# Performance work log

Hardware: AMD Instinct MI355X
Metric: run time of the kernel (lower is better)

Reference implementation:

```python
import jax, jax.numpy as jnp
import numpy as np

N_STEPS = 20
ALPHA, BETA = 0.9, 0.8  # synaptic / membrane decay (unused given zero carried state, kept for clarity)


def _lcn_spiking_layer(h, knn, w, b):
    """h: [N, d_in]; knn: [d_out, K] indices into d_in; w: [d_out, K]; b: [1, d_out].
    Gather K neighbors per output node, weight, reduce, then snntorch Synaptic
    update with zero carried state (the source never stores returned syn/mem):
      syn = ALPHA*0 + I = I ; reset = (prev_mem > thr) = 0 ; mem = BETA*0 + syn - 0 = I
    and the layer output is mem (the source keeps the 3rd return value)."""
    g = h[:, knn]                                  # [N, d_out, K] irregular gather
    cur = jnp.sum(g * w[None, :, :], axis=2) + b   # [N, d_out]
    syn = ALPHA * jnp.zeros_like(cur) + cur
    mem = BETA * jnp.zeros_like(cur) + syn         # reset term is zero
    return mem


def setup_inputs() -> dict:
    key = jax.random.key(0)
    B, T, IN_DIM, K, OUT = 32, N_STEPS, 14400, 25, 2
    dims = [7200, 3600, 1800, 900, 450]
    ks = jax.random.split(key, 13)
    inp = {"x": jax.random.normal(ks[0], (B, T, IN_DIM), dtype=jnp.float32)}
    prev = IN_DIM
    for i, d in enumerate(dims):
        inp[f"w{i}"] = jax.random.normal(ks[1 + i], (d, K), dtype=jnp.float32) * (2.0 / K) ** 0.5
        inp[f"b{i}"] = jnp.zeros((1, d), dtype=jnp.float32)
        inp[f"knn{i}"] = jax.random.randint(ks[6 + i], (d, K), 0, prev)
        prev = d
    inp["Wfc"] = jax.random.normal(ks[11], (dims[-1], OUT), dtype=jnp.float32) * (1.0 / dims[-1]) ** 0.5
    inp["bfc"] = jnp.zeros((OUT,), dtype=jnp.float32)
    return inp


def reference(x, w0, w1, w2, w3, w4, b0, b1, b2, b3, b4, Wfc, bfc,
              knn0, knn1, knn2, knn3, knn4):
    # Source loops over 20 timesteps with independent (state never carried) work;
    # fold time into batch to vectorize, then keep the last step's angle only,
    # exactly matching the returned value of the torch forward.
    B, T, D = x.shape
    h = x.reshape(B * T, D)
    layers = ((w0, b0, knn0), (w1, b1, knn1), (w2, b2, knn2), (w3, b3, knn3), (w4, b4, knn4))
    for w, b, knn in layers:
        h = _lcn_spiking_layer(h, knn, w, b)
    angle = h @ Wfc + bfc                     # [B*T, out_dim]
    angle = angle.reshape(B, T, -1)[:, -1]    # last timestep, as in the source
    return angle
```

## Files before the change

kernel.cpp:

```cpp
#include <hip/hip_runtime.h>
#include <hip/hip_bf16.h>


#define ROWS 32
#define TSTEPS 20
#define D0 14400
#define D1 7200
#define D2 3600
#define D3 1800
#define D4 900
#define D5 450
#define KNB 25

__global__ __launch_bounds__(256)
void l0_stage(const float* __restrict__ x, float* __restrict__ h1t,
              const float* __restrict__ w, const float* __restrict__ bvec,
              const int* __restrict__ knn)
{
    __shared__ float s[D0];
    const int r = blockIdx.y;
    const float* xrow = x + ((size_t)r * TSTEPS + (TSTEPS - 1)) * (size_t)D0;

    const float4* src = reinterpret_cast<const float4*>(xrow);
    float4* dst = reinterpret_cast<float4*>(s);
#pragma unroll 1
    for (int i = threadIdx.x; i < D0 / 4; i += 256)
        dst[i] = src[i];
    __syncthreads();

    const int j0 = blockIdx.x * 900;
#pragma unroll 1
    for (int j = j0 + threadIdx.x; j < j0 + 900; j += 256) {
        const int*   kn = knn + j * KNB;
        const float* ww = w   + j * KNB;
        float acc = bvec[j];
#pragma unroll
        for (int k = 0; k < KNB; ++k)
            acc += s[kn[k]] * ww[k];
        h1t[(j << 5) + r] = acc;
    }
}

__global__ __launch_bounds__(256)
void layer_t_k(const float* __restrict__ pin, float* __restrict__ pout,
               const float* __restrict__ w, const float* __restrict__ bvec,
               const int* __restrict__ knn, int npairs)
{
    const int lane = threadIdx.x & 63;
    const int r  = lane & 31;
    const int jj = lane >> 5;
    const int nw = gridDim.x << 2;
#pragma unroll 1
    for (int jp = (blockIdx.x << 2) + (threadIdx.x >> 6); jp < npairs; jp += nw) {
        const int j = (jp << 1) + jj;
        const int*   kn = knn + j * KNB;
        const float* ww = w   + j * KNB;
        float acc = bvec[j];
#pragma unroll
        for (int k = 0; k < KNB; ++k)
            acc += pin[(kn[k] << 5) + r] * ww[k];
        pout[(j << 5) + r] = acc;
    }
}

__global__ __launch_bounds__(256)
void l4_fc(const float* __restrict__ h4t,
           const float* __restrict__ w, const float* __restrict__ bvec,
           const int* __restrict__ knn,
           const float* __restrict__ Wfc, const float* __restrict__ bfc,
           float* __restrict__ out)
{
    __shared__ float sacc[64];
    if (threadIdx.x < 64)
        sacc[threadIdx.x] = (blockIdx.x == 0) ? bfc[threadIdx.x & 1] : 0.0f;
    __syncthreads();

    const int lane = threadIdx.x & 63;
    const int r  = lane & 31;
    const int jj = lane >> 5;
    const int nw = gridDim.x << 2;
    float c0 = 0.0f, c1 = 0.0f;
#pragma unroll 1
    for (int jp = (blockIdx.x << 2) + (threadIdx.x >> 6); jp < D5 / 2; jp += nw) {
        const int j = (jp << 1) + jj;
        const int*   kn = knn + j * KNB;
        const float* ww = w   + j * KNB;
        float acc = bvec[j];
#pragma unroll
        for (int k = 0; k < KNB; ++k)
            acc += h4t[(kn[k] << 5) + r] * ww[k];
        c0 += acc * Wfc[j * 2 + 0];
        c1 += acc * Wfc[j * 2 + 1];
    }
    atomicAdd(&sacc[(r << 1) + 0], c0);
    atomicAdd(&sacc[(r << 1) + 1], c1);
    __syncthreads();
    if (threadIdx.x < 64)
        atomicAdd(&out[threadIdx.x], sacc[threadIdx.x]);
}

extern "C" void kernel_launch(void* const* d_in, const int* in_sizes, int n_in,
                              void* d_out, int out_size, void* d_ws, size_t ws_size,
                              hipStream_t stream)
{
    const float* x    = (const float*)d_in[0];
    const float* w0   = (const float*)d_in[1];
    const float* b0   = (const float*)d_in[2];
    const int*   knn0 = (const int*)  d_in[3];
    const float* w1   = (const float*)d_in[4];
    const float* b1   = (const float*)d_in[5];
    const int*   knn1 = (const int*)  d_in[6];
    const float* w2   = (const float*)d_in[7];
    const float* b2   = (const float*)d_in[8];
    const int*   knn2 = (const int*)  d_in[9];
    const float* w3   = (const float*)d_in[10];
    const float* b3   = (const float*)d_in[11];
    const int*   knn3 = (const int*)  d_in[12];
    const float* w4   = (const float*)d_in[13];
    const float* b4   = (const float*)d_in[14];
    const int*   knn4 = (const int*)  d_in[15];
    const float* Wfc  = (const float*)d_in[16];
    const float* bfc  = (const float*)d_in[17];
    float* out = (float*)d_out;

    float* h1t = (float*)d_ws;
    float* h2t = h1t + (size_t)D1 * ROWS;
    float* h3t = h2t + (size_t)D2 * ROWS;
    float* h4t = h3t + (size_t)D3 * ROWS;

    hipMemsetAsync(out, 0, (size_t)out_size * sizeof(float), stream);

    l0_stage<<<dim3(D1 / 900, ROWS), dim3(256), 0, stream>>>(x, h1t, w0, b0, knn0);

    layer_t_k<<<dim3(450), dim3(256), 0, stream>>>(h1t, h2t, w1, b1, knn1, D2 / 2);

    layer_t_k<<<dim3(225), dim3(256), 0, stream>>>(h2t, h3t, w2, b2, knn2, D3 / 2);

    layer_t_k<<<dim3(113), dim3(256), 0, stream>>>(h3t, h4t, w3, b3, knn3, D4 / 2);

    l4_fc<<<dim3(57), dim3(256), 0, stream>>>(h4t, w4, b4, knn4, Wfc, bfc, out);
}
```

Measured before the change: 131.0 us.

## Fuse layers one through four and FC into one per-row LDS-resident kernel

Replaces the four tail kernels and the output memset with a single kernel that runs one 1024-thread block per batch row. Every intermediate activation from layer 2 onward lives in shared memory, and the final FC is reduced with wave shuffles. Layer 1 output is now stored row-major so each block can load its row contiguously. This removes launch overhead and global round-trips between layers, but only 32 blocks run, which lowers parallelism, and each block re-reads all the weights and indices.

Result: slower. 138.7 us (+5.9%).

```diff
diff --git a/kernel.cpp b/kernel.cpp
--- a/kernel.cpp
+++ b/kernel.cpp
@@ -1,5 +1,4 @@
 #include <hip/hip_runtime.h>
-#include <hip/hip_bf16.h>
 
 
 #define ROWS 32
@@ -13,7 +12,7 @@
 #define KNB 25
 
 __global__ __launch_bounds__(256)
-void l0_stage(const float* __restrict__ x, float* __restrict__ h1t,
+void l0_stage(const float* __restrict__ x, float* __restrict__ h1,
               const float* __restrict__ w, const float* __restrict__ bvec,
               const int* __restrict__ knn)
 {
@@ -37,66 +36,108 @@
 #pragma unroll
         for (int k = 0; k < KNB; ++k)
             acc += s[kn[k]] * ww[k];
-        h1t[(j << 5) + r] = acc;
+        h1[(size_t)r * D1 + j] = acc;
     }
 }
 
-__global__ __launch_bounds__(256)
-void layer_t_k(const float* __restrict__ pin, float* __restrict__ pout,
-               const float* __restrict__ w, const float* __restrict__ bvec,
-               const int* __restrict__ knn, int npairs)
+__global__ __launch_bounds__(1024)
+void tail_fused(const float* __restrict__ h1,
+                const float* __restrict__ w1, const float* __restrict__ b1, const int* __restrict__ n1,
+                const float* __restrict__ w2, const float* __restrict__ b2, const int* __restrict__ n2,
+                const float* __restrict__ w3, const float* __restrict__ b3, const int* __restrict__ n3,
+                const float* __restrict__ w4, const float* __restrict__ b4, const int* __restrict__ n4,
+                const float* __restrict__ Wfc, const float* __restrict__ bfc,
+                float* __restrict__ out)
 {
-    const int lane = threadIdx.x & 63;
-    const int r  = lane & 31;
-    const int jj = lane >> 5;
-    const int nw = gridDim.x << 2;
+    __shared__ float sa[D1];
+    __shared__ float sb[D2];
+    __shared__ float sc[D3];
+    __shared__ float sd[D4];
+    __shared__ float se[D5];
+    __shared__ float red[2];
+
+    const int r   = blockIdx.x;
+    const int tid = threadIdx.x;
+
+    {
+        const float4* src = reinterpret_cast<const float4*>(h1 + (size_t)r * D1);
+        float4* dst = reinterpret_cast<float4*>(sa);
 #pragma unroll 1
-    for (int jp = (blockIdx.x << 2) + (threadIdx.x >> 6); jp < npairs; jp += nw) {
-        const int j = (jp << 1) + jj;
-        const int*   kn = knn + j * KNB;
-        const float* ww = w   + j * KNB;
-        float acc = bvec[j];
+        for (int i = tid; i < D1 / 4; i += 1024)
+            dst[i] = src[i];
+    }
+    __syncthreads();
+
+#pragma unroll 1
+    for (int j = tid; j < D2; j += 1024) {
+        const int*   kn = n1 + j * KNB;
+        const float* ww = w1 + j * KNB;
+        float acc = b1[j];
 #pragma unroll
         for (int k = 0; k < KNB; ++k)
-            acc += pin[(kn[k] << 5) + r] * ww[k];
-        pout[(j << 5) + r] = acc;
+            acc += sa[kn[k]] * ww[k];
+        sb[j] = acc;
     }
-}
-
-__global__ __launch_bounds__(256)
-void l4_fc(const float* __restrict__ h4t,
-           const float* __restrict__ w, const float* __restrict__ bvec,
-           const int* __restrict__ knn,
-           const float* __restrict__ Wfc, const float* __restrict__ bfc,
-           float* __restrict__ out)
-{
-    __shared__ float sacc[64];
-    if (threadIdx.x < 64)
-        sacc[threadIdx.x] = (blockIdx.x == 0) ? bfc[threadIdx.x & 1] : 0.0f;
     __syncthreads();
 
-    const int lane = threadIdx.x & 63;
-    const int r  = lane & 31;
-    const int jj = lane >> 5;
-    const int nw = gridDim.x << 2;
+#pragma unroll 1
+    for (int j = tid; j < D3; j += 1024) {
+        const int*   kn = n2 + j * KNB;
+        const float* ww = w2 + j * KNB;
+        float acc = b2[j];
+#pragma unroll
+        for (int k = 0; k < KNB; ++k)
+            acc += sb[kn[k]] * ww[k];
+        sc[j] = acc;
+    }
+    __syncthreads();
+
+#pragma unroll 1
+    for (int j = tid; j < D4; j += 1024) {
+        const int*   kn = n3 + j * KNB;
+        const float* ww = w3 + j * KNB;
+        float acc = b3[j];
+#pragma unroll
+        for (int k = 0; k < KNB; ++k)
+            acc += sc[kn[k]] * ww[k];
+        sd[j] = acc;
+    }
+    __syncthreads();
+
+#pragma unroll 1
+    for (int j = tid; j < D5; j += 1024) {
+        const int*   kn = n4 + j * KNB;
+        const float* ww = w4 + j * KNB;
+        float acc = b4[j];
+#pragma unroll
+        for (int k = 0; k < KNB; ++k)
+            acc += sd[kn[k]] * ww[k];
+        se[j] = acc;
+    }
+    __syncthreads();
+
+    if (tid == 0) { red[0] = bfc[0]; red[1] = bfc[1]; }
+
     float c0 = 0.0f, c1 = 0.0f;
 #pragma unroll 1
-    for (int jp = (blockIdx.x << 2) + (threadIdx.x >> 6); jp < D5 / 2; jp += nw) {
-        const int j = (jp << 1) + jj;
-        const int*   kn = knn + j * KNB;
-        const float* ww = w   + j * KNB;
-        float acc = bvec[j];
+    for (int j = tid; j < D5; j += 1024) {
+        const float v = se[j];
+        c0 += v * Wfc[2 * j + 0];
+        c1 += v * Wfc[2 * j + 1];
+    }
 #pragma unroll
-        for (int k = 0; k < KNB; ++k)
-            acc += h4t[(kn[k] << 5) + r] * ww[k];
-        c0 += acc * Wfc[j * 2 + 0];
-        c1 += acc * Wfc[j * 2 + 1];
+    for (int off = 32; off > 0; off >>= 1) {
+        c0 += __shfl_down(c0, off);
+        c1 += __shfl_down(c1, off);
     }
-    atomicAdd(&sacc[(r << 1) + 0], c0);
-    atomicAdd(&sacc[(r << 1) + 1], c1);
     __syncthreads();
-    if (threadIdx.x < 64)
-        atomicAdd(&out[threadIdx.x], sacc[threadIdx.x]);
+    if ((tid & 63) == 0) {
+        atomicAdd(&red[0], c0);
+        atomicAdd(&red[1], c1);
+    }
+    __syncthreads();
+    if (tid < 2)
+        out[2 * r + tid] = red[tid];
 }
 
 extern "C" void kernel_launch(void* const* d_in, const int* in_sizes, int n_in,
@@ -123,20 +164,15 @@
     const float* bfc  = (const float*)d_in[17];
     float* out = (float*)d_out;
 
-    float* h1t = (float*)d_ws;
-    float* h2t = h1t + (size_t)D1 * ROWS;
-    float* h3t = h2t + (size_t)D2 * ROWS;
-    float* h4t = h3t + (size_t)D3 * ROWS;
+    float* h1 = (float*)d_ws;
 
-    hipMemsetAsync(out, 0, (size_t)out_size * sizeof(float), stream);
+    l0_stage<<<dim3(D1 / 900, ROWS), dim3(256), 0, stream>>>(x, h1, w0, b0, knn0);
 
-    l0_stage<<<dim3(D1 / 900, ROWS), dim3(256), 0, stream>>>(x, h1t, w0, b0, knn0);
-
-    layer_t_k<<<dim3(450), dim3(256), 0, stream>>>(h1t, h2t, w1, b1, knn1, D2 / 2);
-
-    layer_t_k<<<dim3(225), dim3(256), 0, stream>>>(h2t, h3t, w2, b2, knn2, D3 / 2);
-
-    layer_t_k<<<dim3(113), dim3(256), 0, stream>>>(h3t, h4t, w3, b3, knn3, D4 / 2);
-
-    l4_fc<<<dim3(57), dim3(256), 0, stream>>>(h4t, w4, b4, knn4, Wfc, bfc, out);
+    tail_fused<<<dim3(ROWS), dim3(1024), 0, stream>>>(
+        h1,
+        w1, b1, knn1,
+        w2, b2, knn2,
+        w3, b3, knn3,
+        w4, b4, knn4,
+        Wfc, bfc, out);
 }
```
